# Performance work log

Hardware: AMD Instinct MI355X
Metric: run time of the kernel (lower is better)

Reference implementation:

```python
import jax, jax.numpy as jnp
import numpy as np

N = 32768          # total proposals (batch of images concatenated)
C = 81             # num classes (class 0 = background)
K = 4096           # fixed candidate budget for masked NMS (jit-friendly)
SCORE_THRESH = 0.05
NMS_THRESH = 0.5
IMG_W, IMG_H = 1333.0, 800.0   # image size for clip_to_image
CLS_OFFSET = 4096.0            # > max coord: offsets boxes per label so NMS is per-class


def setup_inputs() -> dict:
    key = jax.random.key(0)
    k1, k2, k3 = jax.random.split(key, 3)
    x = jax.random.normal(k1, (N, C), dtype=jnp.float32)
    xy = jax.random.uniform(k2, (N, 2), dtype=jnp.float32) * jnp.array([IMG_W * 0.9, IMG_H * 0.9], jnp.float32)
    wh = 4.0 + jax.random.uniform(k3, (N, 2), dtype=jnp.float32) * 124.0
    boxes = jnp.concatenate([xy, xy + wh], axis=-1)  # [N,4] xyxy
    return {"x": x, "boxes": boxes}


def _pairwise_iou(b):
    # b: [K,4] xyxy -> [K,K] IoU
    x1, y1, x2, y2 = b[:, 0], b[:, 1], b[:, 2], b[:, 3]
    area = (x2 - x1) * (y2 - y1)
    iw = jnp.maximum(jnp.minimum(x2[:, None], x2[None, :]) - jnp.maximum(x1[:, None], x1[None, :]), 0.0)
    ih = jnp.maximum(jnp.minimum(y2[:, None], y2[None, :]) - jnp.maximum(y1[:, None], y1[None, :]), 0.0)
    inter = iw * ih
    return inter / (area[:, None] + area[None, :] - inter + 1e-9)


def reference(x, boxes):
    # softmax scores
    prob = jax.nn.softmax(x, axis=-1)                    # [N,C]
    # clip_to_image (remove_empty=False)
    bx = jnp.stack([
        jnp.clip(boxes[:, 0], 0.0, IMG_W - 1),
        jnp.clip(boxes[:, 1], 0.0, IMG_H - 1),
        jnp.clip(boxes[:, 2], 0.0, IMG_W - 1),
        jnp.clip(boxes[:, 3], 0.0, IMG_H - 1)], axis=-1)  # [N,4]
    # score threshold + drop background (label 0), as in filter_results
    valid = (prob > SCORE_THRESH) & (jnp.arange(C)[None, :] != 0)
    flat = jnp.where(valid, prob, -1.0).reshape(-1)       # [N*C]
    vals, idx = jax.lax.top_k(flat, K)                    # sorted desc
    box_idx = idx // C
    labels = idx % C                                      # [K] int
    bk = bx[box_idx]                                      # [K,4] (boxes repeated per class in torch code)
    keep0 = vals > 0.0                                    # invalid slots padded with -1
    # multi-label NMS: offset boxes by label so different classes never overlap
    boff = bk + (labels.astype(bk.dtype) * CLS_OFFSET)[:, None]
    iou_gt = _pairwise_iou(boff) > NMS_THRESH             # [K,K] bool
    order = jnp.arange(K)

    def step(keep, i):
        sup = keep[i] & (order > i) & iou_gt[i]
        return keep & ~sup, None

    keep, _ = jax.lax.scan(step, keep0, order)
    dets = jnp.where(keep[:, None],
                     jnp.concatenate([bk, vals[:, None]], axis=-1),
                     0.0)                                 # [K,5] = xyxy + score
    return dets, labels, keep
```

## Files before the change

### kernel.cpp

```cpp
#include <hip/hip_runtime.h>

#pragma clang fp contract(off)

typedef unsigned int u32;
typedef unsigned long long u64;
typedef long long i64;

#define N_ROWS 32768
#define NCLS 81
#define TOPK 4096
#define IMGW_M1 1332.0f
#define IMGH_M1 799.0f

#define CAND_THREADS 256
#define RPB 32
#define CAND_GRID (N_ROWS / RPB)
#define CPT 11
#define BLK_CAND_CAP 640
#define ROW_F4 ((RPB * NCLS) / 4)

#define H1_BASE 0x3D4Cu
#define H1_BINS 576

#define NSLICE 32
#define SUBCAP 384
#define SEG_LDS 4096

#define MCAP 1024
#define MMAX 512
#define NW32 16

__device__ inline double fast_exp_neg(double d) {
    if (d < -45.0) return 0.0;
    const double L2E    = 1.4426950408889634074;
    const double LN2_HI = 6.93147180369123816490e-01;
    const double LN2_LO = 1.90821492927058770002e-10;
    double n = __builtin_rint(d * L2E);
    double r = __builtin_fma(-n, LN2_HI, d);
    r = __builtin_fma(-n, LN2_LO, r);
    double p = 1.0 / 6227020800.0;
    p = __builtin_fma(p, r, 1.0 / 479001600.0);
    p = __builtin_fma(p, r, 1.0 / 39916800.0);
    p = __builtin_fma(p, r, 1.0 / 3628800.0);
    p = __builtin_fma(p, r, 1.0 / 362880.0);
    p = __builtin_fma(p, r, 1.0 / 40320.0);
    p = __builtin_fma(p, r, 1.0 / 5040.0);
    p = __builtin_fma(p, r, 1.0 / 720.0);
    p = __builtin_fma(p, r, 1.0 / 120.0);
    p = __builtin_fma(p, r, 1.0 / 24.0);
    p = __builtin_fma(p, r, 1.0 / 6.0);
    p = __builtin_fma(p, r, 0.5);
    p = __builtin_fma(p, r, 1.0);
    p = __builtin_fma(p, r, 1.0);
    i64 ni = (i64)n;
    double sc = __longlong_as_double((i64)(1023 + ni) << 52);
    return p * sc;
}

__global__ void __launch_bounds__(256) k_cand(const float* __restrict__ x,
                                              u32* __restrict__ binCur,
                                              u64* __restrict__ selBins) {
    __shared__ float4 lx4[ROW_F4];
    __shared__ u32 lK[BLK_CAND_CAP];
    __shared__ u32 lI[BLK_CAND_CAP];
    __shared__ u32 lcnt;
    float* lx = (float*)lx4;
    const int t = threadIdx.x;
    if (t == 0) lcnt = 0;

    const float4* xv = (const float4*)x + (size_t)blockIdx.x * ROW_F4;
    for (int i = t; i < ROW_F4; i += CAND_THREADS) lx4[i] = xv[i];
    __syncthreads();

    const int rl = t >> 3;
    const int q = t & 7;
    const int c0 = q * 10;
    const int cEff = (q == 7) ? 11 : 10;
    const int row = blockIdx.x * RPB + rl;
    const float* xr = lx + rl * NCLS;

    float v[CPT];
    #pragma unroll
    for (int i = 0; i < CPT; i++) v[i] = (i < cEff) ? xr[c0 + i] : -1.0e30f;

    float m = v[0];
    #pragma unroll
    for (int i = 1; i < CPT; i++) m = fmaxf(m, v[i]);
    m = fmaxf(m, __shfl_xor(m, 1));
    m = fmaxf(m, __shfl_xor(m, 2));
    m = fmaxf(m, __shfl_xor(m, 4));

    double e[CPT];
    #pragma unroll
    for (int i = 0; i < CPT; i++) {
        if (i < cEff) {
            float d = v[i] - m;
            e[i] = fast_exp_neg((double)d);
        } else e[i] = 0.0;
    }
    double s = 0.0;
    #pragma unroll
    for (int i = 0; i < CPT; i++) if (i < cEff) s += e[i];
    s += __shfl_xor(s, 1);
    s += __shfl_xor(s, 2);
    s += __shfl_xor(s, 4);

    const double THRMID = (double)0.05f + 0x1.0p-29;
    double ethr = THRMID * s;
    #pragma unroll
    for (int i = 0; i < CPT; i++) {
        int c = c0 + i;
        if (i < cEff && c != 0 && e[i] > ethr) {
            float pf = (float)(e[i] / s);
            u32 slot = atomicAdd(&lcnt, 1u);
            lK[slot] = __float_as_uint(pf);
            lI[slot] = (u32)(row * NCLS + c);
        }
    }
    __syncthreads();

    const u32 tot = lcnt;
    const u32 sbase = (blockIdx.x & (NSLICE - 1)) * H1_BINS;
    for (u32 i = t; i < tot; i += CAND_THREADS) {
        u32 key = lK[i];
        u32 b = (key >> 16) - H1_BASE;
        u32 pos = atomicAdd(&binCur[sbase + b], 1u);
        if (pos < (u32)SUBCAP)
            selBins[(size_t)(sbase + b) * SUBCAP + pos] =
                ((u64)key << 32) | (u64)(0xFFFFFFFFu - lI[i]);
    }
}

__global__ void __launch_bounds__(256) k_binrank(const u64* __restrict__ selBins,
                                                 const u32* __restrict__ binCur,
                                                 const float* __restrict__ boxes,
                                                 float* __restrict__ rboxes,
                                                 float* __restrict__ rvals,
                                                 int* __restrict__ rlabel,
                                                 float* __restrict__ out) {
    __shared__ u32 cs[1040];
    __shared__ u64 seg[SEG_LDS];
    __shared__ u32 sBase[NSLICE + 1];
    __shared__ u32 Bsh;
    const int t = threadIdx.x;

    if (t == 0) Bsh = 0;

    {
        u32 s0 = 0, s1 = 0, s2 = 0;
        const bool g1 = (t + 256) < H1_BINS;
        const bool g2 = (t + 512) < H1_BINS;
        #pragma unroll 4
        for (int j = 0; j < NSLICE; j++) {
            const u32* hp = binCur + j * H1_BINS;
            s0 += hp[t];
            if (g1) s1 += hp[t + 256];
            if (g2) s2 += hp[t + 512];
        }
        cs[t] = s0;
        cs[t + 256] = g1 ? s1 : 0u;
        cs[t + 512] = g2 ? s2 : 0u;
        cs[t + 768] = 0u;
    }
    __syncthreads();
    for (int d = 1; d < 1024; d <<= 1) {
        u32 a0 = (t + d < 1024) ? cs[t + d] : 0u;
        u32 a1 = (t + 256 + d < 1024) ? cs[t + 256 + d] : 0u;
        u32 a2 = (t + 512 + d < 1024) ? cs[t + 512 + d] : 0u;
        u32 a3 = (t + 768 + d < 1024) ? cs[t + 768 + d] : 0u;
        __syncthreads();
        cs[t] += a0; cs[t + 256] += a1; cs[t + 512] += a2; cs[t + 768] += a3;
        __syncthreads();
    }
    #pragma unroll
    for (int qq = 0; qq < 3; qq++) {
        int i = t + qq * 256;
        if (i < H1_BINS) {
            if (cs[i] >= (u32)TOPK && cs[i + 1] < (u32)TOPK) Bsh = (u32)i;
        }
    }
    __syncthreads();
    const u32 B = Bsh;

    if (blockIdx.x == H1_BINS) {
        u32 covered = cs[B];
        if (covered > (u32)TOPK) covered = TOPK;
        for (u32 r = covered + t; r < TOPK; r += 256) {
            rboxes[r * 4 + 0] = 0; rboxes[r * 4 + 1] = 0;
            rboxes[r * 4 + 2] = 0; rboxes[r * 4 + 3] = 0;
            rvals[r] = 0.0f; rlabel[r] = 0;
            out[TOPK * 5 + r] = 0.0f;
            out[TOPK * 6 + r] = 0.0f;
            float* d = out + (size_t)r * 5;
            d[0] = 0; d[1] = 0; d[2] = 0; d[3] = 0; d[4] = 0;
        }
        return;
    }

    const u32 b = blockIdx.x;
    if (b < B) return;
    u32 start = cs[b + 1];
    u32 end = cs[b];
    if (start >= end) return;
    if (start >= (u32)TOPK) return;

    if (t < NSLICE) {
        u32 c0s = binCur[t * H1_BINS + b];
        if (c0s > (u32)SUBCAP) c0s = SUBCAP;
        u32 inc = c0s;
        #pragma unroll
        for (int d = 1; d < NSLICE; d <<= 1) {
            u32 o = __shfl_up(inc, d);
            if (t >= d) inc += o;
        }
        sBase[t] = inc - c0s;
        if (t == NSLICE - 1) sBase[NSLICE] = inc;
    }
    __syncthreads();
    const u32 lenSt = sBase[NSLICE];
    const u32 ldsLen = lenSt < (u32)SEG_LDS ? lenSt : (u32)SEG_LDS;
    {
        const u32 s = (u32)t >> 3;
        const u32 base = sBase[s];
        const u32 cntS = sBase[s + 1] - base;
        const u64* gs = selBins + ((size_t)s * H1_BINS + b) * SUBCAP;
        for (u32 i = (u32)t & 7u; i < cntS; i += 8u) {
            u32 d = base + i;
            if (d < (u32)SEG_LDS) seg[d] = gs[i];
        }
    }
    __syncthreads();

    for (u32 i = t; i < ldsLen; i += 256) {
        u64 c = seg[i];
        u32 r0 = 0;
        for (u32 j = 0; j < ldsLen; j++) r0 += (seg[j] > c) ? 1u : 0u;
        u32 r = start + r0;
        if (r >= (u32)TOPK) continue;
        u32 idx = 0xFFFFFFFFu - (u32)(c & 0xFFFFFFFFull);
        float val = __uint_as_float((u32)(c >> 32));
        u32 bi = idx / NCLS;
        u32 lab = idx % NCLS;
        const float* bp = boxes + (size_t)bi * 4;
        float x1 = fminf(fmaxf(bp[0], 0.0f), IMGW_M1);
        float y1 = fminf(fmaxf(bp[1], 0.0f), IMGH_M1);
        float x2 = fminf(fmaxf(bp[2], 0.0f), IMGW_M1);
        float y2 = fminf(fmaxf(bp[3], 0.0f), IMGH_M1);
        rboxes[r * 4 + 0] = x1; rboxes[r * 4 + 1] = y1;
        rboxes[r * 4 + 2] = x2; rboxes[r * 4 + 3] = y2;
        rvals[r] = val;
        rlabel[r] = (int)lab;
        out[TOPK * 5 + r] = (float)lab;
    }
}

__device__ inline float4 nms_box(u32 g, const float4* __restrict__ boxL,
                                 const float* __restrict__ rboxes,
                                 const unsigned short* __restrict__ memRank, float off) {
    if (g < (u32)MCAP) return boxL[g];
    float4 b = ((const float4*)rboxes)[memRank[g]];
    return make_float4(b.x + off, b.y + off, b.z + off, b.w + off);
}
__device__ inline float nms_area(u32 g, const float* __restrict__ areaL, float4 b) {
    if (g < (u32)MCAP) return areaL[g];
    return (b.z - b.x) * (b.w - b.y);
}

__global__ void __launch_bounds__(256) k_nms(const float* __restrict__ rboxes,
                                             const float* __restrict__ rvals,
                                             const int* __restrict__ rlabel,
                                             float* __restrict__ out) {
    int c = blockIdx.x + 1;
    __shared__ int lLab[TOPK];
    __shared__ float4 boxL[MCAP];
    __shared__ float areaL[MCAP];
    __shared__ unsigned short memRank[TOPK];
    __shared__ u32 colW[MMAX * NW32];
    __shared__ u32 remOut[NW32];
    __shared__ unsigned char keepL[TOPK];
    __shared__ u32 cc[64];
    __shared__ u32 baseC[64];
    __shared__ u32 mTotSh;
    const int t = threadIdx.x;
    const int w = t >> 6, lane = t & 63;
    const u64 laneLT = ((u64)1 << lane) - 1;
    const float off = (float)c * 4096.0f;

    {
        const int4* g4 = (const int4*)rlabel;
        int4* l4 = (int4*)lLab;
        for (int i = t; i < TOPK / 4; i += 256) l4[i] = g4[i];
    }
    __syncthreads();

    for (int it = 0; it < 16; it++) {
        int chunk = it * 4 + w;
        int r = chunk * 64 + lane;
        u64 mask = __ballot(lLab[r] == c);
        if (lane == 0) cc[chunk] = (u32)__popcll(mask);
    }
    __syncthreads();
    if (t < 64) {
        u32 v = cc[t];
        u32 inc = v;
        #pragma unroll
        for (int d = 1; d < 64; d <<= 1) {
            u32 o = __shfl_up(inc, d);
            if (lane >= d) inc += o;
        }
        baseC[t] = inc - v;
        if (t == 63) mTotSh = inc;
    }
    __syncthreads();
    const u32 m = mTotSh;
    for (int it = 0; it < 16; it++) {
        int chunk = it * 4 + w;
        int r = chunk * 64 + lane;
        bool match = (lLab[r] == c);
        u64 mask = __ballot(match);
        if (match) {
            u32 g = baseC[chunk] + (u32)__popcll(mask & laneLT);
            memRank[g] = (unsigned short)r;
            if (g < (u32)MCAP) {
                float4 b = ((const float4*)rboxes)[r];
                float bx1 = b.x + off, by1 = b.y + off;
                float bx2 = b.z + off, by2 = b.w + off;
                boxL[g] = make_float4(bx1, by1, bx2, by2);
                areaL[g] = (bx2 - bx1) * (by2 - by1);
            }
        }
    }
    __syncthreads();

    const bool matrixPath = (m <= (u32)MMAX);
    if (matrixPath) {
        const u32 nW = (m + 31) >> 5;
        const u32 items = m * nW;
        for (u32 p = t; p < items; p += 256) {
            u32 s = p / nW;
            u32 wd = p - s * nW;
            float4 bs = nms_box(s, boxL, rboxes, memRank, off);
            float as = nms_area(s, areaL, bs);
            u32 word = 0;
            u32 j0 = wd << 5;
            u32 jend = j0 + 32; if (jend > m) jend = m;
            u32 js = (j0 > s + 1) ? j0 : (s + 1);
            for (u32 j = js; j < jend; j++) {
                float4 bj = nms_box(j, boxL, rboxes, memRank, off);
                float aj = nms_area(j, areaL, bj);
                float iw = fmaxf(fminf(bs.z, bj.z) - fmaxf(bs.x, bj.x), 0.0f);
                float ih = fmaxf(fminf(bs.w, bj.w) - fmaxf(bs.y, bj.y), 0.0f);
                float inter = iw * ih;
                float iou = inter / (as + aj - inter + 1e-9f);
                if (iou > 0.5f) word |= (1u << (j - j0));
            }
            colW[s * NW32 + wd] = word;
        }
        __syncthreads();
        if (t < 64) {
            u32 remW = 0;
            bool own = ((u32)lane < ((m + 31) >> 5));
            for (u32 s2 = 0; s2 < m; s2++) {
                u32 rw = __shfl(remW, (int)(s2 >> 5));
                bool removed = (rw >> (s2 & 31)) & 1u;
                u32 cw = own ? colW[s2 * NW32 + lane] : 0u;
                if (!removed) remW |= cw;
            }
            if (own) remOut[lane] = remW;
        }
        __syncthreads();
    } else {
        for (u32 q2 = t; q2 < m; q2 += 256) keepL[q2] = 1;
        __syncthreads();
        for (u32 i = 0; i < m; i++) {
            __syncthreads();
            if (!keepL[i]) continue;
            float4 bi = nms_box(i, boxL, rboxes, memRank, off);
            float ai = nms_area(i, areaL, bi);
            for (u32 jj = i + 1 + t; jj < m; jj += 256) {
                if (!keepL[jj]) continue;
                float4 bj = nms_box(jj, boxL, rboxes, memRank, off);
                float aj = nms_area(jj, areaL, bj);
                float iw = fmaxf(fminf(bi.z, bj.z) - fmaxf(bi.x, bj.x), 0.0f);
                float ih = fmaxf(fminf(bi.w, bj.w) - fmaxf(bi.y, bj.y), 0.0f);
                float inter = iw * ih;
                float iou = inter / (ai + aj - inter + 1e-9f);
                if (iou > 0.5f) keepL[jj] = 0;
            }
        }
        __syncthreads();
    }

    for (u32 q2 = t; q2 < m; q2 += 256) {
        bool keep = matrixPath ? !((remOut[q2 >> 5] >> (q2 & 31)) & 1u)
                               : (keepL[q2] != 0);
        int r = memRank[q2];
        out[TOPK * 6 + r] = keep ? 1.0f : 0.0f;
        float* d = out + (size_t)r * 5;
        if (keep) {
            float4 b = ((const float4*)rboxes)[r];
            d[0] = b.x; d[1] = b.y; d[2] = b.z; d[3] = b.w;
            d[4] = rvals[r];
        } else {
            d[0] = 0; d[1] = 0; d[2] = 0; d[3] = 0; d[4] = 0;
        }
    }
}

extern "C" void kernel_launch(void* const* d_in, const int* in_sizes, int n_in,
                              void* d_out, int out_size, void* d_ws, size_t ws_size,
                              hipStream_t stream) {
    const float* x = (const float*)d_in[0];
    const float* boxes = (const float*)d_in[1];
    float* out = (float*)d_out;

    u32* W = (u32*)d_ws;
    u32* binCur = W;
    u64* selBins = (u64*)((char*)d_ws + 131072);
    float* rboxes = (float*)(selBins + (size_t)NSLICE * H1_BINS * SUBCAP);
    float* rvals = rboxes + 4 * TOPK;
    int* rlabel = (int*)(rvals + TOPK);

    hipMemsetAsync(binCur, 0, NSLICE * H1_BINS * sizeof(u32), stream);
    k_cand<<<CAND_GRID, CAND_THREADS, 0, stream>>>(x, binCur, selBins);
    k_binrank<<<H1_BINS + 1, 256, 0, stream>>>(selBins, binCur, boxes,
                                               rboxes, rvals, rlabel, out);
    k_nms<<<80, 256, 0, stream>>>(rboxes, rvals, rlabel, out);
}
```

Measured before the change: 107.9 us.

## Fuse bin-rank and per-class NMS into one persistent kernel with grid barrier

Merges the bin-ranking kernel and the per-class NMS kernel into a single 384-block kernel. Blocks loop over histogram bins in a grid-stride fashion, then meet at a software grid barrier (atomic counter plus spin) before 80 of them run per-class NMS. One kernel launch and the boundary between them go away, and the LDS buffers are shared through one aliased scratch array. The matrix-path NMS also drops its global-memory fallback for box loads and reads class labels straight from global memory. In exchange, the barrier relies on all 384 blocks being co-resident, and some blocks now rank two bins one after the other.

```diff
diff --git a/kernel.cpp b/kernel.cpp
--- a/kernel.cpp
+++ b/kernel.cpp
@@ -26,9 +26,11 @@
 #define SUBCAP 384
 #define SEG_LDS 4096
 
+#define RBN_BLK 384
 #define MCAP 1024
 #define MMAX 512
 #define NW32 16
+#define SMEM_BYTES 61440
 
 __device__ inline double fast_exp_neg(double d) {
     if (d < -45.0) return 0.0;
@@ -57,6 +59,23 @@
     return p * sc;
 }
 
+__device__ inline void grid_barrier(u32* bar, u32 idx, u32 nblk) {
+    __syncthreads();
+    if (threadIdx.x == 0) {
+        __threadfence();
+        __hip_atomic_fetch_add(&bar[idx], 1u, __ATOMIC_ACQ_REL,
+                               __HIP_MEMORY_SCOPE_AGENT);
+        u32 spins = 0;
+        while (__hip_atomic_load(&bar[idx], __ATOMIC_ACQUIRE,
+                                 __HIP_MEMORY_SCOPE_AGENT) < nblk) {
+            __builtin_amdgcn_s_sleep(8);
+            if (++spins > 4000000u) break;
+        }
+        __threadfence();
+    }
+    __syncthreads();
+}
+
 __global__ void __launch_bounds__(256) k_cand(const float* __restrict__ x,
                                               u32* __restrict__ binCur,
                                               u64* __restrict__ selBins) {
@@ -131,278 +150,284 @@
     }
 }
 
-__global__ void __launch_bounds__(256) k_binrank(const u64* __restrict__ selBins,
-                                                 const u32* __restrict__ binCur,
-                                                 const float* __restrict__ boxes,
-                                                 float* __restrict__ rboxes,
-                                                 float* __restrict__ rvals,
-                                                 int* __restrict__ rlabel,
-                                                 float* __restrict__ out) {
-    __shared__ u32 cs[1040];
-    __shared__ u64 seg[SEG_LDS];
+__global__ void __launch_bounds__(256) k_rbn(const u64* __restrict__ selBins,
+                                             const u32* __restrict__ binCur,
+                                             const float* __restrict__ boxes,
+                                             u32* __restrict__ bar,
+                                             float* __restrict__ rboxes,
+                                             float* __restrict__ rvals,
+                                             int* __restrict__ rlabel,
+                                             float* __restrict__ out) {
+    __shared__ __align__(16) unsigned char smem[SMEM_BYTES];
+    __shared__ u32 Bsh;
     __shared__ u32 sBase[NSLICE + 1];
-    __shared__ u32 Bsh;
-    const int t = threadIdx.x;
-
-    if (t == 0) Bsh = 0;
-
-    {
-        u32 s0 = 0, s1 = 0, s2 = 0;
-        const bool g1 = (t + 256) < H1_BINS;
-        const bool g2 = (t + 512) < H1_BINS;
-        #pragma unroll 4
-        for (int j = 0; j < NSLICE; j++) {
-            const u32* hp = binCur + j * H1_BINS;
-            s0 += hp[t];
-            if (g1) s1 += hp[t + 256];
-            if (g2) s2 += hp[t + 512];
-        }
-        cs[t] = s0;
-        cs[t + 256] = g1 ? s1 : 0u;
-        cs[t + 512] = g2 ? s2 : 0u;
-        cs[t + 768] = 0u;
-    }
-    __syncthreads();
-    for (int d = 1; d < 1024; d <<= 1) {
-        u32 a0 = (t + d < 1024) ? cs[t + d] : 0u;
-        u32 a1 = (t + 256 + d < 1024) ? cs[t + 256 + d] : 0u;
-        u32 a2 = (t + 512 + d < 1024) ? cs[t + 512 + d] : 0u;
-        u32 a3 = (t + 768 + d < 1024) ? cs[t + 768 + d] : 0u;
-        __syncthreads();
-        cs[t] += a0; cs[t + 256] += a1; cs[t + 512] += a2; cs[t + 768] += a3;
-        __syncthreads();
-    }
-    #pragma unroll
-    for (int qq = 0; qq < 3; qq++) {
-        int i = t + qq * 256;
-        if (i < H1_BINS) {
-            if (cs[i] >= (u32)TOPK && cs[i + 1] < (u32)TOPK) Bsh = (u32)i;
-        }
-    }
-    __syncthreads();
-    const u32 B = Bsh;
-
-    if (blockIdx.x == H1_BINS) {
-        u32 covered = cs[B];
-        if (covered > (u32)TOPK) covered = TOPK;
-        for (u32 r = covered + t; r < TOPK; r += 256) {
-            rboxes[r * 4 + 0] = 0; rboxes[r * 4 + 1] = 0;
-            rboxes[r * 4 + 2] = 0; rboxes[r * 4 + 3] = 0;
-            rvals[r] = 0.0f; rlabel[r] = 0;
-            out[TOPK * 5 + r] = 0.0f;
-            out[TOPK * 6 + r] = 0.0f;
-            float* d = out + (size_t)r * 5;
-            d[0] = 0; d[1] = 0; d[2] = 0; d[3] = 0; d[4] = 0;
-        }
-        return;
-    }
-
-    const u32 b = blockIdx.x;
-    if (b < B) return;
-    u32 start = cs[b + 1];
-    u32 end = cs[b];
-    if (start >= end) return;
-    if (start >= (u32)TOPK) return;
-
-    if (t < NSLICE) {
-        u32 c0s = binCur[t * H1_BINS + b];
-        if (c0s > (u32)SUBCAP) c0s = SUBCAP;
-        u32 inc = c0s;
-        #pragma unroll
-        for (int d = 1; d < NSLICE; d <<= 1) {
-            u32 o = __shfl_up(inc, d);
-            if (t >= d) inc += o;
-        }
-        sBase[t] = inc - c0s;
-        if (t == NSLICE - 1) sBase[NSLICE] = inc;
-    }
-    __syncthreads();
-    const u32 lenSt = sBase[NSLICE];
-    const u32 ldsLen = lenSt < (u32)SEG_LDS ? lenSt : (u32)SEG_LDS;
-    {
-        const u32 s = (u32)t >> 3;
-        const u32 base = sBase[s];
-        const u32 cntS = sBase[s + 1] - base;
-        const u64* gs = selBins + ((size_t)s * H1_BINS + b) * SUBCAP;
-        for (u32 i = (u32)t & 7u; i < cntS; i += 8u) {
-            u32 d = base + i;
-            if (d < (u32)SEG_LDS) seg[d] = gs[i];
-        }
-    }
-    __syncthreads();
-
-    for (u32 i = t; i < ldsLen; i += 256) {
-        u64 c = seg[i];
-        u32 r0 = 0;
-        for (u32 j = 0; j < ldsLen; j++) r0 += (seg[j] > c) ? 1u : 0u;
-        u32 r = start + r0;
-        if (r >= (u32)TOPK) continue;
-        u32 idx = 0xFFFFFFFFu - (u32)(c & 0xFFFFFFFFull);
-        float val = __uint_as_float((u32)(c >> 32));
-        u32 bi = idx / NCLS;
-        u32 lab = idx % NCLS;
-        const float* bp = boxes + (size_t)bi * 4;
-        float x1 = fminf(fmaxf(bp[0], 0.0f), IMGW_M1);
-        float y1 = fminf(fmaxf(bp[1], 0.0f), IMGH_M1);
-        float x2 = fminf(fmaxf(bp[2], 0.0f), IMGW_M1);
-        float y2 = fminf(fmaxf(bp[3], 0.0f), IMGH_M1);
-        rboxes[r * 4 + 0] = x1; rboxes[r * 4 + 1] = y1;
-        rboxes[r * 4 + 2] = x2; rboxes[r * 4 + 3] = y2;
-        rvals[r] = val;
-        rlabel[r] = (int)lab;
-        out[TOPK * 5 + r] = (float)lab;
-    }
-}
-
-__device__ inline float4 nms_box(u32 g, const float4* __restrict__ boxL,
-                                 const float* __restrict__ rboxes,
-                                 const unsigned short* __restrict__ memRank, float off) {
-    if (g < (u32)MCAP) return boxL[g];
-    float4 b = ((const float4*)rboxes)[memRank[g]];
-    return make_float4(b.x + off, b.y + off, b.z + off, b.w + off);
-}
-__device__ inline float nms_area(u32 g, const float* __restrict__ areaL, float4 b) {
-    if (g < (u32)MCAP) return areaL[g];
-    return (b.z - b.x) * (b.w - b.y);
-}
-
-__global__ void __launch_bounds__(256) k_nms(const float* __restrict__ rboxes,
-                                             const float* __restrict__ rvals,
-                                             const int* __restrict__ rlabel,
-                                             float* __restrict__ out) {
-    int c = blockIdx.x + 1;
-    __shared__ int lLab[TOPK];
-    __shared__ float4 boxL[MCAP];
-    __shared__ float areaL[MCAP];
-    __shared__ unsigned short memRank[TOPK];
-    __shared__ u32 colW[MMAX * NW32];
-    __shared__ u32 remOut[NW32];
-    __shared__ unsigned char keepL[TOPK];
     __shared__ u32 cc[64];
     __shared__ u32 baseC[64];
+    __shared__ u32 remOut[NW32];
     __shared__ u32 mTotSh;
     const int t = threadIdx.x;
-    const int w = t >> 6, lane = t & 63;
-    const u64 laneLT = ((u64)1 << lane) - 1;
-    const float off = (float)c * 4096.0f;
+    const u32 bid = blockIdx.x;
 
     {
-        const int4* g4 = (const int4*)rlabel;
-        int4* l4 = (int4*)lLab;
-        for (int i = t; i < TOPK / 4; i += 256) l4[i] = g4[i];
-    }
-    __syncthreads();
-
-    for (int it = 0; it < 16; it++) {
-        int chunk = it * 4 + w;
-        int r = chunk * 64 + lane;
-        u64 mask = __ballot(lLab[r] == c);
-        if (lane == 0) cc[chunk] = (u32)__popcll(mask);
-    }
-    __syncthreads();
-    if (t < 64) {
-        u32 v = cc[t];
-        u32 inc = v;
+        u32* cs = (u32*)smem;
+        u64* seg = (u64*)(smem + 4160);
+
+        if (t == 0) Bsh = 0;
+        {
+            u32 s0 = 0, s1 = 0, s2 = 0;
+            const bool g1 = (t + 256) < H1_BINS;
+            const bool g2 = (t + 512) < H1_BINS;
+            #pragma unroll 4
+            for (int j = 0; j < NSLICE; j++) {
+                const u32* hp = binCur + j * H1_BINS;
+                s0 += hp[t];
+                if (g1) s1 += hp[t + 256];
+                if (g2) s2 += hp[t + 512];
+            }
+            cs[t] = s0;
+            cs[t + 256] = g1 ? s1 : 0u;
+            cs[t + 512] = g2 ? s2 : 0u;
+            cs[t + 768] = 0u;
+        }
+        __syncthreads();
+        for (int d = 1; d < 1024; d <<= 1) {
+            u32 a0 = (t + d < 1024) ? cs[t + d] : 0u;
+            u32 a1 = (t + 256 + d < 1024) ? cs[t + 256 + d] : 0u;
+            u32 a2 = (t + 512 + d < 1024) ? cs[t + 512 + d] : 0u;
+            u32 a3 = (t + 768 + d < 1024) ? cs[t + 768 + d] : 0u;
+            __syncthreads();
+            cs[t] += a0; cs[t + 256] += a1; cs[t + 512] += a2; cs[t + 768] += a3;
+            __syncthreads();
+        }
         #pragma unroll
-        for (int d = 1; d < 64; d <<= 1) {
-            u32 o = __shfl_up(inc, d);
-            if (lane >= d) inc += o;
-        }
-        baseC[t] = inc - v;
-        if (t == 63) mTotSh = inc;
-    }
-    __syncthreads();
-    const u32 m = mTotSh;
-    for (int it = 0; it < 16; it++) {
-        int chunk = it * 4 + w;
-        int r = chunk * 64 + lane;
-        bool match = (lLab[r] == c);
-        u64 mask = __ballot(match);
-        if (match) {
-            u32 g = baseC[chunk] + (u32)__popcll(mask & laneLT);
-            memRank[g] = (unsigned short)r;
-            if (g < (u32)MCAP) {
-                float4 b = ((const float4*)rboxes)[r];
-                float bx1 = b.x + off, by1 = b.y + off;
-                float bx2 = b.z + off, by2 = b.w + off;
-                boxL[g] = make_float4(bx1, by1, bx2, by2);
-                areaL[g] = (bx2 - bx1) * (by2 - by1);
-            }
-        }
-    }
-    __syncthreads();
-
-    const bool matrixPath = (m <= (u32)MMAX);
-    if (matrixPath) {
-        const u32 nW = (m + 31) >> 5;
-        const u32 items = m * nW;
-        for (u32 p = t; p < items; p += 256) {
-            u32 s = p / nW;
-            u32 wd = p - s * nW;
-            float4 bs = nms_box(s, boxL, rboxes, memRank, off);
-            float as = nms_area(s, areaL, bs);
-            u32 word = 0;
-            u32 j0 = wd << 5;
-            u32 jend = j0 + 32; if (jend > m) jend = m;
-            u32 js = (j0 > s + 1) ? j0 : (s + 1);
-            for (u32 j = js; j < jend; j++) {
-                float4 bj = nms_box(j, boxL, rboxes, memRank, off);
-                float aj = nms_area(j, areaL, bj);
-                float iw = fmaxf(fminf(bs.z, bj.z) - fmaxf(bs.x, bj.x), 0.0f);
-                float ih = fmaxf(fminf(bs.w, bj.w) - fmaxf(bs.y, bj.y), 0.0f);
-                float inter = iw * ih;
-                float iou = inter / (as + aj - inter + 1e-9f);
-                if (iou > 0.5f) word |= (1u << (j - j0));
-            }
-            colW[s * NW32 + wd] = word;
+        for (int qq = 0; qq < 3; qq++) {
+            int i = t + qq * 256;
+            if (i < H1_BINS) {
+                if (cs[i] >= (u32)TOPK && cs[i + 1] < (u32)TOPK) Bsh = (u32)i;
+            }
+        }
+        __syncthreads();
+        const u32 B = Bsh;
+
+        for (int bb = (int)bid; bb <= H1_BINS; bb += RBN_BLK) {
+            if (bb == H1_BINS) {
+                u32 covered = cs[B];
+                if (covered > (u32)TOPK) covered = TOPK;
+                for (u32 r = covered + (u32)t; r < (u32)TOPK; r += 256) {
+                    rboxes[r * 4 + 0] = 0; rboxes[r * 4 + 1] = 0;
+                    rboxes[r * 4 + 2] = 0; rboxes[r * 4 + 3] = 0;
+                    rvals[r] = 0.0f; rlabel[r] = 0;
+                    out[TOPK * 5 + r] = 0.0f;
+                    out[TOPK * 6 + r] = 0.0f;
+                    float* d = out + (size_t)r * 5;
+                    d[0] = 0; d[1] = 0; d[2] = 0; d[3] = 0; d[4] = 0;
+                }
+                continue;
+            }
+            const u32 b = (u32)bb;
+            if (b < B) continue;
+            u32 start = cs[b + 1];
+            u32 end = cs[b];
+            if (start >= end) continue;
+            if (start >= (u32)TOPK) continue;
+
+            __syncthreads();
+            if (t < NSLICE) {
+                u32 c0s = binCur[t * H1_BINS + b];
+                if (c0s > (u32)SUBCAP) c0s = SUBCAP;
+                u32 inc = c0s;
+                #pragma unroll
+                for (int d = 1; d < NSLICE; d <<= 1) {
+                    u32 o = __shfl_up(inc, d);
+                    if (t >= d) inc += o;
+                }
+                sBase[t] = inc - c0s;
+                if (t == NSLICE - 1) sBase[NSLICE] = inc;
+            }
+            __syncthreads();
+            const u32 lenSt = sBase[NSLICE];
+            const u32 ldsLen = lenSt < (u32)SEG_LDS ? lenSt : (u32)SEG_LDS;
+            {
+                const u32 s = (u32)t >> 3;
+                const u32 base = sBase[s];
+                const u32 cntS = sBase[s + 1] - base;
+                const u64* gs = selBins + ((size_t)s * H1_BINS + b) * SUBCAP;
+                for (u32 i = (u32)t & 7u; i < cntS; i += 8u) {
+                    u32 d = base + i;
+                    if (d < (u32)SEG_LDS) seg[d] = gs[i];
+                }
+            }
+            __syncthreads();
+
+            for (u32 i = (u32)t; i < ldsLen; i += 256) {
+                u64 c = seg[i];
+                u32 r0 = 0;
+                for (u32 j = 0; j < ldsLen; j++) r0 += (seg[j] > c) ? 1u : 0u;
+                u32 r = start + r0;
+                if (r >= (u32)TOPK) continue;
+                u32 idx = 0xFFFFFFFFu - (u32)(c & 0xFFFFFFFFull);
+                float val = __uint_as_float((u32)(c >> 32));
+                u32 bi = idx / NCLS;
+                u32 lab = idx % NCLS;
+                const float* bp = boxes + (size_t)bi * 4;
+                float x1 = fminf(fmaxf(bp[0], 0.0f), IMGW_M1);
+                float y1 = fminf(fmaxf(bp[1], 0.0f), IMGH_M1);
+                float x2 = fminf(fmaxf(bp[2], 0.0f), IMGW_M1);
+                float y2 = fminf(fmaxf(bp[3], 0.0f), IMGH_M1);
+                rboxes[r * 4 + 0] = x1; rboxes[r * 4 + 1] = y1;
+                rboxes[r * 4 + 2] = x2; rboxes[r * 4 + 3] = y2;
+                rvals[r] = val;
+                rlabel[r] = (int)lab;
+                out[TOPK * 5 + r] = (float)lab;
+            }
+        }
+    }
+
+    grid_barrier(bar, 0, RBN_BLK);
+    if (bid >= 80) return;
+
+    {
+        float4* boxL = (float4*)smem;
+        float* areaL = (float*)(smem + 16384);
+        unsigned short* memRank = (unsigned short*)(smem + 20480);
+        u32* colW = (u32*)(smem + 28672);
+        unsigned char* keepL = (unsigned char*)(smem + 28672);
+
+        int c = (int)bid + 1;
+        const int w = t >> 6, lane = t & 63;
+        const u64 laneLT = ((u64)1 << lane) - 1;
+        const float off = (float)c * 4096.0f;
+
+        for (int it = 0; it < 16; it++) {
+            int chunk = it * 4 + w;
+            int r = chunk * 64 + lane;
+            u64 mask = __ballot(rlabel[r] == c);
+            if (lane == 0) cc[chunk] = (u32)__popcll(mask);
         }
         __syncthreads();
         if (t < 64) {
-            u32 remW = 0;
-            bool own = ((u32)lane < ((m + 31) >> 5));
-            for (u32 s2 = 0; s2 < m; s2++) {
-                u32 rw = __shfl(remW, (int)(s2 >> 5));
-                bool removed = (rw >> (s2 & 31)) & 1u;
-                u32 cw = own ? colW[s2 * NW32 + lane] : 0u;
-                if (!removed) remW |= cw;
-            }
-            if (own) remOut[lane] = remW;
+            u32 v = cc[t];
+            u32 inc = v;
+            #pragma unroll
+            for (int d = 1; d < 64; d <<= 1) {
+                u32 o = __shfl_up(inc, d);
+                if (lane >= d) inc += o;
+            }
+            baseC[t] = inc - v;
+            if (t == 63) mTotSh = inc;
         }
         __syncthreads();
-    } else {
-        for (u32 q2 = t; q2 < m; q2 += 256) keepL[q2] = 1;
+        const u32 m = mTotSh;
+        for (int it = 0; it < 16; it++) {
+            int chunk = it * 4 + w;
+            int r = chunk * 64 + lane;
+            bool match = (rlabel[r] == c);
+            u64 mask = __ballot(match);
+            if (match) {
+                u32 g = baseC[chunk] + (u32)__popcll(mask & laneLT);
+                memRank[g] = (unsigned short)r;
+                if (g < (u32)MCAP) {
+                    float4 b = ((const float4*)rboxes)[r];
+                    float bx1 = b.x + off, by1 = b.y + off;
+                    float bx2 = b.z + off, by2 = b.w + off;
+                    boxL[g] = make_float4(bx1, by1, bx2, by2);
+                    areaL[g] = (bx2 - bx1) * (by2 - by1);
+                }
+            }
+        }
         __syncthreads();
-        for (u32 i = 0; i < m; i++) {
-            __syncthreads();
-            if (!keepL[i]) continue;
-            float4 bi = nms_box(i, boxL, rboxes, memRank, off);
-            float ai = nms_area(i, areaL, bi);
-            for (u32 jj = i + 1 + t; jj < m; jj += 256) {
-                if (!keepL[jj]) continue;
-                float4 bj = nms_box(jj, boxL, rboxes, memRank, off);
-                float aj = nms_area(jj, areaL, bj);
-                float iw = fmaxf(fminf(bi.z, bj.z) - fmaxf(bi.x, bj.x), 0.0f);
-                float ih = fmaxf(fminf(bi.w, bj.w) - fmaxf(bi.y, bj.y), 0.0f);
-                float inter = iw * ih;
-                float iou = inter / (ai + aj - inter + 1e-9f);
-                if (iou > 0.5f) keepL[jj] = 0;
-            }
-        }
-        __syncthreads();
-    }
-
-    for (u32 q2 = t; q2 < m; q2 += 256) {
-        bool keep = matrixPath ? !((remOut[q2 >> 5] >> (q2 & 31)) & 1u)
-                               : (keepL[q2] != 0);
-        int r = memRank[q2];
-        out[TOPK * 6 + r] = keep ? 1.0f : 0.0f;
-        float* d = out + (size_t)r * 5;
-        if (keep) {
-            float4 b = ((const float4*)rboxes)[r];
-            d[0] = b.x; d[1] = b.y; d[2] = b.z; d[3] = b.w;
-            d[4] = rvals[r];
+
+        const bool matrixPath = (m <= (u32)MMAX);
+        if (matrixPath) {
+            const u32 nW = (m + 31) >> 5;
+            const u32 items = m * nW;
+            for (u32 p = (u32)t; p < items; p += 256) {
+                u32 s = p / nW;
+                u32 wd = p - s * nW;
+                float4 bs = (s < (u32)MCAP) ? boxL[s]
+                    : make_float4(0.f, 0.f, 0.f, 0.f);
+                float as = (s < (u32)MCAP) ? areaL[s] : 0.f;
+                u32 word = 0;
+                u32 j0 = wd << 5;
+                u32 jend = j0 + 32; if (jend > m) jend = m;
+                u32 js = (j0 > s + 1) ? j0 : (s + 1);
+                for (u32 j = js; j < jend; j++) {
+                    float4 bj = boxL[j];
+                    float aj = areaL[j];
+                    float iw = fmaxf(fminf(bs.z, bj.z) - fmaxf(bs.x, bj.x), 0.0f);
+                    float ih = fmaxf(fminf(bs.w, bj.w) - fmaxf(bs.y, bj.y), 0.0f);
+                    float inter = iw * ih;
+                    float iou = inter / (as + aj - inter + 1e-9f);
+                    if (iou > 0.5f) word |= (1u << (j - j0));
+                }
+                colW[s * NW32 + wd] = word;
+            }
+            __syncthreads();
+            if (t < 64) {
+                u32 remW = 0;
+                bool own = ((u32)lane < ((m + 31) >> 5));
+                for (u32 s2 = 0; s2 < m; s2++) {
+                    u32 rw = __shfl(remW, (int)(s2 >> 5));
+                    bool removed = (rw >> (s2 & 31)) & 1u;
+                    u32 cw = own ? colW[s2 * NW32 + lane] : 0u;
+                    if (!removed) remW |= cw;
+                }
+                if (own) remOut[lane] = remW;
+            }
+            __syncthreads();
         } else {
-            d[0] = 0; d[1] = 0; d[2] = 0; d[3] = 0; d[4] = 0;
+            for (u32 q2 = (u32)t; q2 < m; q2 += 256) keepL[q2] = 1;
+            __syncthreads();
+            for (u32 i = 0; i < m; i++) {
+                __syncthreads();
+                if (!keepL[i]) continue;
+                float4 bi;
+                float ai;
+                {
+                    u32 g = i;
+                    if (g < (u32)MCAP) { bi = boxL[g]; ai = areaL[g]; }
+                    else {
+                        float4 bb2 = ((const float4*)rboxes)[memRank[g]];
+                        bi = make_float4(bb2.x + off, bb2.y + off,
+                                         bb2.z + off, bb2.w + off);
+                        ai = (bi.z - bi.x) * (bi.w - bi.y);
+                    }
+                }
+                for (u32 jj = i + 1 + (u32)t; jj < m; jj += 256) {
+                    if (!keepL[jj]) continue;
+                    float4 bj;
+                    float aj;
+                    u32 g = jj;
+                    if (g < (u32)MCAP) { bj = boxL[g]; aj = areaL[g]; }
+                    else {
+                        float4 bb2 = ((const float4*)rboxes)[memRank[g]];
+                        bj = make_float4(bb2.x + off, bb2.y + off,
+                                         bb2.z + off, bb2.w + off);
+                        aj = (bj.z - bj.x) * (bj.w - bj.y);
+                    }
+                    float iw = fmaxf(fminf(bi.z, bj.z) - fmaxf(bi.x, bj.x), 0.0f);
+                    float ih = fmaxf(fminf(bi.w, bj.w) - fmaxf(bi.y, bj.y), 0.0f);
+                    float inter = iw * ih;
+                    float iou = inter / (ai + aj - inter + 1e-9f);
+                    if (iou > 0.5f) keepL[jj] = 0;
+                }
+            }
+            __syncthreads();
+        }
+
+        for (u32 q2 = (u32)t; q2 < m; q2 += 256) {
+            bool keep = matrixPath ? !((remOut[q2 >> 5] >> (q2 & 31)) & 1u)
+                                   : (keepL[q2] != 0);
+            int r = memRank[q2];
+            out[TOPK * 6 + r] = keep ? 1.0f : 0.0f;
+            float* d = out + (size_t)r * 5;
+            if (keep) {
+                float4 b = ((const float4*)rboxes)[r];
+                d[0] = b.x; d[1] = b.y; d[2] = b.z; d[3] = b.w;
+                d[4] = rvals[r];
+            } else {
+                d[0] = 0; d[1] = 0; d[2] = 0; d[3] = 0; d[4] = 0;
+            }
         }
     }
 }
@@ -415,15 +440,15 @@
     float* out = (float*)d_out;
 
     u32* W = (u32*)d_ws;
-    u32* binCur = W;
+    u32* bar = W;
+    u32* binCur = W + 16;
     u64* selBins = (u64*)((char*)d_ws + 131072);
     float* rboxes = (float*)(selBins + (size_t)NSLICE * H1_BINS * SUBCAP);
     float* rvals = rboxes + 4 * TOPK;
     int* rlabel = (int*)(rvals + TOPK);
 
-    hipMemsetAsync(binCur, 0, NSLICE * H1_BINS * sizeof(u32), stream);
+    hipMemsetAsync(W, 0, (16 + NSLICE * H1_BINS) * sizeof(u32), stream);
     k_cand<<<CAND_GRID, CAND_THREADS, 0, stream>>>(x, binCur, selBins);
-    k_binrank<<<H1_BINS + 1, 256, 0, stream>>>(selBins, binCur, boxes,
-                                               rboxes, rvals, rlabel, out);
-    k_nms<<<80, 256, 0, stream>>>(rboxes, rvals, rlabel, out);
+    k_rbn<<<RBN_BLK, 256, 0, stream>>>(selBins, binCur, boxes, bar,
+                                       rboxes, rvals, rlabel, out);
 }
```

Result: slower. 150.3 us (+39.2%).

## Sub-bucket bin candidates by secondary key byte before rank counting

Applied to the files above, without the earlier changes.

Within each first-level histogram bin, candidates are now counting-sorted into 256 sub-buckets keyed on the next 8 bits of the score key, using an LDS histogram, a suffix scan and a scatter. Each candidate then counts greater elements only inside its own sub-bucket, and the sub-bucket offset supplies the rest of its rank. This replaces the quadratic all-pairs rank scan over the whole bin. In exchange it adds a second global read pass, LDS atomics and an 8-step scan with barriers.

```diff
diff --git a/kernel.cpp b/kernel.cpp
--- a/kernel.cpp
+++ b/kernel.cpp
@@ -140,6 +140,8 @@
                                                  float* __restrict__ out) {
     __shared__ u32 cs[1040];
     __shared__ u64 seg[SEG_LDS];
+    __shared__ u32 h2[256];
+    __shared__ u32 cur2[256];
     __shared__ u32 sBase[NSLICE + 1];
     __shared__ u32 Bsh;
     const int t = threadIdx.x;
@@ -216,25 +218,51 @@
         sBase[t] = inc - c0s;
         if (t == NSLICE - 1) sBase[NSLICE] = inc;
     }
+    h2[t] = 0;
+    cur2[t] = 0;
     __syncthreads();
     const u32 lenSt = sBase[NSLICE];
     const u32 ldsLen = lenSt < (u32)SEG_LDS ? lenSt : (u32)SEG_LDS;
+
     {
         const u32 s = (u32)t >> 3;
-        const u32 base = sBase[s];
-        const u32 cntS = sBase[s + 1] - base;
+        const u32 cntS = sBase[s + 1] - sBase[s];
         const u64* gs = selBins + ((size_t)s * H1_BINS + b) * SUBCAP;
         for (u32 i = (u32)t & 7u; i < cntS; i += 8u) {
-            u32 d = base + i;
-            if (d < (u32)SEG_LDS) seg[d] = gs[i];
-        }
-    }
-    __syncthreads();
-
-    for (u32 i = t; i < ldsLen; i += 256) {
+            u32 s2 = (u32)(gs[i] >> 40) & 0xFFu;
+            atomicAdd(&h2[s2], 1u);
+        }
+    }
+    __syncthreads();
+    for (int d = 1; d < 256; d <<= 1) {
+        u32 o = (t + d < 256) ? h2[t + d] : 0u;
+        __syncthreads();
+        h2[t] += o;
+        __syncthreads();
+    }
+
+    {
+        const u32 s = (u32)t >> 3;
+        const u32 cntS = sBase[s + 1] - sBase[s];
+        const u64* gs = selBins + ((size_t)s * H1_BINS + b) * SUBCAP;
+        for (u32 i = (u32)t & 7u; i < cntS; i += 8u) {
+            u64 c = gs[i];
+            u32 s2 = (u32)(c >> 40) & 0xFFu;
+            u32 lo = (s2 < 255u) ? h2[s2 + 1] : 0u;
+            u32 pos = lo + atomicAdd(&cur2[s2], 1u);
+            if (pos < (u32)SEG_LDS) seg[pos] = c;
+        }
+    }
+    __syncthreads();
+
+    for (u32 i = (u32)t; i < ldsLen; i += 256) {
         u64 c = seg[i];
-        u32 r0 = 0;
-        for (u32 j = 0; j < ldsLen; j++) r0 += (seg[j] > c) ? 1u : 0u;
+        u32 s2 = (u32)(c >> 40) & 0xFFu;
+        u32 lo = (s2 < 255u) ? h2[s2 + 1] : 0u;
+        u32 hi = h2[s2];
+        if (hi > ldsLen) hi = ldsLen;
+        u32 r0 = lo;
+        for (u32 j = lo; j < hi; j++) r0 += (seg[j] > c) ? 1u : 0u;
         u32 r = start + r0;
         if (r >= (u32)TOPK) continue;
         u32 idx = 0xFFFFFFFFu - (u32)(c & 0xFFFFFFFFull);
```

Result: no change. 109.7 us (+1.6%).

## Compute global histogram prefix once in last candidate block

Applied to the files above, without the earlier changes.

Moves the cross-slice histogram reduction and suffix scan out of every k_binrank block and into the last-finishing k_cand block, detected with an atomic done counter and fences. The scan result and the threshold bin are written to global memory, and k_binrank reads them instead of recomputing. This removes 577 redundant reductions over 32 slices plus the scans. The cost is a serialized tail in k_cand, where only one block does the scan, and extra LDS use in k_cand, which may lower occupancy.

```diff
diff --git a/kernel.cpp b/kernel.cpp
--- a/kernel.cpp
+++ b/kernel.cpp
@@ -59,14 +59,19 @@
 
 __global__ void __launch_bounds__(256) k_cand(const float* __restrict__ x,
                                               u32* __restrict__ binCur,
-                                              u64* __restrict__ selBins) {
+                                              u64* __restrict__ selBins,
+                                              u32* __restrict__ doneCnt,
+                                              u32* __restrict__ sufG) {
     __shared__ float4 lx4[ROW_F4];
     __shared__ u32 lK[BLK_CAND_CAP];
     __shared__ u32 lI[BLK_CAND_CAP];
+    __shared__ u32 cs[1040];
     __shared__ u32 lcnt;
+    __shared__ u32 lastSh;
+    __shared__ u32 Bsh;
     float* lx = (float*)lx4;
     const int t = threadIdx.x;
-    if (t == 0) lcnt = 0;
+    if (t == 0) { lcnt = 0; Bsh = 0; }
 
     const float4* xv = (const float4*)x + (size_t)blockIdx.x * ROW_F4;
     for (int i = t; i < ROW_F4; i += CAND_THREADS) lx4[i] = xv[i];
@@ -129,22 +134,17 @@
             selBins[(size_t)(sbase + b) * SUBCAP + pos] =
                 ((u64)key << 32) | (u64)(0xFFFFFFFFu - lI[i]);
     }
-}
-
-__global__ void __launch_bounds__(256) k_binrank(const u64* __restrict__ selBins,
-                                                 const u32* __restrict__ binCur,
-                                                 const float* __restrict__ boxes,
-                                                 float* __restrict__ rboxes,
-                                                 float* __restrict__ rvals,
-                                                 int* __restrict__ rlabel,
-                                                 float* __restrict__ out) {
-    __shared__ u32 cs[1040];
-    __shared__ u64 seg[SEG_LDS];
-    __shared__ u32 sBase[NSLICE + 1];
-    __shared__ u32 Bsh;
-    const int t = threadIdx.x;
-
-    if (t == 0) Bsh = 0;
+    __syncthreads();
+
+    if (t == 0) {
+        __threadfence();
+        u32 tk = __hip_atomic_fetch_add(doneCnt, 1u, __ATOMIC_ACQ_REL,
+                                        __HIP_MEMORY_SCOPE_AGENT);
+        lastSh = (tk == (u32)(CAND_GRID - 1)) ? 1u : 0u;
+        if (lastSh) __threadfence();
+    }
+    __syncthreads();
+    if (!lastSh) return;
 
     {
         u32 s0 = 0, s1 = 0, s2 = 0;
@@ -180,10 +180,27 @@
         }
     }
     __syncthreads();
-    const u32 B = Bsh;
+    sufG[t] = cs[t];
+    sufG[t + 256] = cs[t + 256];
+    if (t + 512 <= H1_BINS) sufG[t + 512] = cs[t + 512];
+    if (t == 0) sufG[577] = Bsh;
+}
+
+__global__ void __launch_bounds__(256) k_binrank(const u64* __restrict__ selBins,
+                                                 const u32* __restrict__ binCur,
+                                                 const u32* __restrict__ sufG,
+                                                 const float* __restrict__ boxes,
+                                                 float* __restrict__ rboxes,
+                                                 float* __restrict__ rvals,
+                                                 int* __restrict__ rlabel,
+                                                 float* __restrict__ out) {
+    __shared__ u64 seg[SEG_LDS];
+    __shared__ u32 sBase[NSLICE + 1];
+    const int t = threadIdx.x;
+    const u32 B = sufG[577];
 
     if (blockIdx.x == H1_BINS) {
-        u32 covered = cs[B];
+        u32 covered = sufG[B];
         if (covered > (u32)TOPK) covered = TOPK;
         for (u32 r = covered + t; r < TOPK; r += 256) {
             rboxes[r * 4 + 0] = 0; rboxes[r * 4 + 1] = 0;
@@ -199,8 +216,8 @@
 
     const u32 b = blockIdx.x;
     if (b < B) return;
-    u32 start = cs[b + 1];
-    u32 end = cs[b];
+    u32 start = sufG[b + 1];
+    u32 end = sufG[b];
     if (start >= end) return;
     if (start >= (u32)TOPK) return;
 
@@ -231,7 +248,7 @@
     }
     __syncthreads();
 
-    for (u32 i = t; i < ldsLen; i += 256) {
+    for (u32 i = (u32)t; i < ldsLen; i += 256) {
         u64 c = seg[i];
         u32 r0 = 0;
         for (u32 j = 0; j < ldsLen; j++) r0 += (seg[j] > c) ? 1u : 0u;
@@ -415,15 +432,17 @@
     float* out = (float*)d_out;
 
     u32* W = (u32*)d_ws;
-    u32* binCur = W;
+    u32* doneCnt = W;
+    u32* sufG = W + 16;
+    u32* binCur = W + 1024;
     u64* selBins = (u64*)((char*)d_ws + 131072);
     float* rboxes = (float*)(selBins + (size_t)NSLICE * H1_BINS * SUBCAP);
     float* rvals = rboxes + 4 * TOPK;
     int* rlabel = (int*)(rvals + TOPK);
 
-    hipMemsetAsync(binCur, 0, NSLICE * H1_BINS * sizeof(u32), stream);
-    k_cand<<<CAND_GRID, CAND_THREADS, 0, stream>>>(x, binCur, selBins);
-    k_binrank<<<H1_BINS + 1, 256, 0, stream>>>(selBins, binCur, boxes,
+    hipMemsetAsync(W, 0, 4096 + NSLICE * H1_BINS * sizeof(u32), stream);
+    k_cand<<<CAND_GRID, CAND_THREADS, 0, stream>>>(x, binCur, selBins, doneCnt, sufG);
+    k_binrank<<<H1_BINS + 1, 256, 0, stream>>>(selBins, binCur, sufG, boxes,
                                                rboxes, rvals, rlabel, out);
     k_nms<<<80, 256, 0, stream>>>(rboxes, rvals, rlabel, out);
 }
```

New measurement: 158.3 us. 1.47x slower.
